# Performance work log

Hardware: AMD Instinct MI355X
Metric: run time of the kernel (lower is better)

The kernel has to match this reference:

```python
import jax, jax.numpy as jnp
import numpy as np

SG_SLOPE = 20.0  # fast_sigmoid surrogate slope
THRESHOLD = 1.0

@jax.custom_vjp
def spike_fn(v):
    # Heaviside spike with fast-sigmoid surrogate gradient
    return (v > 0).astype(v.dtype)

def _spike_fwd(v):
    return spike_fn(v), v

def _spike_bwd(v, g):
    return (g / (SG_SLOPE * jnp.abs(v) + 1.0) ** 2,)

spike_fn.defvjp(_spike_fwd, _spike_bwd)

def setup_inputs() -> dict:
    key = jax.random.key(0)
    T, IN, H, HEADS, O = 8192, 192, 1024, 5, 2
    dt = 0.004
    sp = float(np.log1p(np.exp(0.5413)))  # softplus(param) ~= 1.0
    tau_syn_h, tau_mem_h = 0.01 * sp, 0.02 * sp
    tau_syn_r = np.array([0.01, 0.02, 0.05, 0.1, 0.2]) * sp
    tau_mem_r = np.array([0.02, 0.05, 0.1, 0.2, 0.5]) * sp
    k1, k2, k3, k4 = jax.random.split(key, 4)
    x = jax.random.normal(k1, (T, IN), jnp.float32)
    W_in = jax.random.normal(k2, (H, IN), jnp.float32) / np.sqrt(IN)
    V = jax.random.normal(k3, (H, H), jnp.float32) / np.sqrt(H)
    b_rec = jnp.zeros((H,), jnp.float32)
    W_out = jax.random.normal(k4, (HEADS, O, H), jnp.float32) / np.sqrt(H)
    return {
        "x": x, "W_in": W_in, "V": V, "b_rec": b_rec, "W_out": W_out,
        "alpha_h": jnp.float32(np.exp(-dt / tau_syn_h)),
        "beta_h": jnp.float32(np.exp(-dt / tau_mem_h)),
        "alpha_r": jnp.asarray(np.exp(-dt / tau_syn_r), jnp.float32),
        "beta_r": jnp.asarray(np.exp(-dt / tau_mem_r), jnp.float32),
    }

def reference(x, W_in, V, b_rec, W_out, alpha_h, beta_h, alpha_r, beta_r):
    H = W_in.shape[0]
    HEADS, O, _ = W_out.shape
    dt_f32 = x.dtype

    def step(carry, x_t):
        inp_prev, spk, syn_h, mem_h, syn_r, mem_r = carry
        # hidden RSynaptic (note: fc_hidden consumes the PREVIOUS input, one-step delay)
        cur = W_in @ inp_prev + V @ spk + b_rec
        syn_h_new = alpha_h * syn_h + cur
        reset = jax.lax.stop_gradient(spk)  # zero-reset uses previous spike, detached
        mem_h_new = (beta_h * mem_h + syn_h_new) * (1.0 - reset)
        spk_new = spike_fn(mem_h_new - THRESHOLD)
        # readout heads consume the PREVIOUS hidden spike (pre-update)
        r_in = jnp.einsum("hoc,c->ho", W_out, spk)  # [HEADS, 2]
        syn_r_new = alpha_r[:, None] * syn_r + r_in
        mem_r_new = beta_r[:, None] * mem_r + syn_r_new  # reset_mechanism='none'
        out = mem_r_new.mean(axis=0)  # average over readout heads
        return (x_t, spk_new, syn_h_new, mem_h_new, syn_r_new, mem_r_new), out

    init = (
        jnp.zeros_like(x[0]),
        jnp.zeros((H,), dt_f32),
        jnp.zeros((H,), dt_f32),
        jnp.zeros((H,), dt_f32),
        jnp.zeros((HEADS, O), dt_f32),
        jnp.zeros((HEADS, O), dt_f32),
    )
    _, preds = jax.lax.scan(step, init, x)
    return preds  # [T, 2]
```

## Files before the change

kernel.cpp:

```cpp
#include <hip/hip_runtime.h>
#include <hip/hip_bf16.h>


constexpr int T_STEPS = 8192;
constexpr int IN_DIM  = 192;
constexpr int H_DIM   = 1024;
constexpr int NBLK    = 32;
constexpr int RING    = 4;

__global__ void k_clear(unsigned int* __restrict__ p, int n) {
    int i = blockIdx.x * blockDim.x + threadIdx.x;
    if (i < n) p[i] = 0u;
}

__global__ __launch_bounds__(576, 1) void k_phase1(
    const float* __restrict__ x,
    const float* __restrict__ W_in,
    const float* __restrict__ V,
    const float* __restrict__ b_rec,
    const float* __restrict__ alpha_h_p,
    const float* __restrict__ beta_h_p,
    unsigned long long* __restrict__ mbox,
    uint2* __restrict__ raster)
{
    const int tid   = threadIdx.x;
    const int blk   = blockIdx.x;
    const int w     = tid >> 6;
    const int l     = tid & 63;
    const bool syncw = (w == 8);
    const int r_local = l >> 4;
    const int cg      = l & 15;
    const int row   = (blk << 5) + (w << 2) + r_local;

    __shared__ unsigned int       bits_lds[RING][NBLK];
    __shared__ unsigned long long combine[2];
    __shared__ unsigned long long rdyPack;

    for (int i = tid; i < RING * NBLK; i += 576)
        ((unsigned int*)bits_lds)[i] = 0u;
    if (tid == 0) { combine[0] = 0ull; combine[1] = 0ull; rdyPack = 0ull; }

    unsigned int* rp = (unsigned int*)&rdyPack;

    float4 vfrag[16];
    float  wfrag[12];
    float  b_r = 0.f;
    if (!syncw) {
        const float4* vp = (const float4*)(V + (size_t)row * H_DIM + cg * 64);
        #pragma unroll
        for (int i = 0; i < 16; ++i) vfrag[i] = vp[i];
        const float* wp = W_in + row * IN_DIM + cg * 12;
        #pragma unroll
        for (int i = 0; i < 12; ++i) wfrag[i] = wp[i];
        b_r = b_rec[row];
    }
    const float ah = alpha_h_p[0];
    const float bh = beta_h_p[0];

    __syncthreads();

    float u0 = 1.02f, u1 = 1.03f, u2 = 1.05f, u3 = 1.07f;
    const float bc = 1.0000001f, bd = 1e-30f;

    if (syncw) {
        const bool act = (l < NBLK) && (l != blk);
        for (int t = 0; t < T_STEPS - 1; ++t) {
            const unsigned int want = (unsigned int)(t + 1);
            const unsigned long long good =
                ((unsigned long long)want << 16) | ((unsigned long long)want << 48);
            const unsigned long long* p =
                &mbox[(size_t)(((t & (RING - 1)) * NBLK + blk) * NBLK + l)];
            unsigned long long vv = act
                ? __hip_atomic_load(p, __ATOMIC_RELAXED, __HIP_MEMORY_SCOPE_AGENT)
                : good;
            bool ok = (((vv >> 16) & 0xffffull) == want) && ((vv >> 48) == want);
            while (__any(!ok)) {
                if (!ok)
                    vv = __hip_atomic_load(p, __ATOMIC_RELAXED,
                                           __HIP_MEMORY_SCOPE_AGENT);
                #pragma unroll
                for (int i = 0; i < 8; ++i) {
                    u0 = fmaf(u0, bc, bd); u1 = fmaf(u1, bc, bd);
                    u2 = fmaf(u2, bc, bd); u3 = fmaf(u3, bc, bd);
                }
                ok = (((vv >> 16) & 0xffffull) == want) && ((vv >> 48) == want);
            }
            if (act)
                bits_lds[t & (RING - 1)][l] =
                    (unsigned int)(vv & 0xffffull)
                    | ((unsigned int)((vv >> 32) & 0xffffull) << 16);
            if (l == 0)
                __hip_atomic_store(&rp[0], (unsigned int)(t + 1),
                                   __ATOMIC_RELEASE, __HIP_MEMORY_SCOPE_WORKGROUP);
        }
    } else {
        const float* xptr = x + cg * 12;
        float xr[12];
        #pragma unroll
        for (int i = 0; i < 12; ++i) xr[i] = 0.0f;
        float syn = 0.f, mem = 0.f, prev = 0.f;

        for (int t = 0; t < T_STEPS; ++t) {
            const float4* xp4 = (const float4*)xptr;
            float4 f0 = xp4[0], f1 = xp4[1], f2 = xp4[2];

            unsigned long long rv = __hip_atomic_load(&rdyPack, __ATOMIC_ACQUIRE,
                                        __HIP_MEMORY_SCOPE_WORKGROUP);
            while ((unsigned int)rv < (unsigned int)t ||
                   (unsigned int)(rv >> 32) < (unsigned int)t) {
                #pragma unroll
                for (int i = 0; i < 4; ++i) {
                    u0 = fmaf(u0, bc, bd); u1 = fmaf(u1, bc, bd);
                    u2 = fmaf(u2, bc, bd); u3 = fmaf(u3, bc, bd);
                }
                rv = __hip_atomic_load(&rdyPack, __ATOMIC_ACQUIRE,
                                       __HIP_MEMORY_SCOPE_WORKGROUP);
            }

            const int slot = (t + RING - 1) & (RING - 1);
            unsigned int b0 = bits_lds[slot][2 * cg];
            unsigned int b1 = bits_lds[slot][2 * cg + 1];

            float a0 = 0.f, a1 = 0.f;
            #pragma unroll
            for (int i = 0; i < 8; ++i) {
                a0 = fmaf((float)((b0 >> (4 * i + 0)) & 1u), vfrag[i].x, a0);
                a0 = fmaf((float)((b0 >> (4 * i + 1)) & 1u), vfrag[i].y, a0);
                a0 = fmaf((float)((b0 >> (4 * i + 2)) & 1u), vfrag[i].z, a0);
                a0 = fmaf((float)((b0 >> (4 * i + 3)) & 1u), vfrag[i].w, a0);
                a1 = fmaf((float)((b1 >> (4 * i + 0)) & 1u), vfrag[8 + i].x, a1);
                a1 = fmaf((float)((b1 >> (4 * i + 1)) & 1u), vfrag[8 + i].y, a1);
                a1 = fmaf((float)((b1 >> (4 * i + 2)) & 1u), vfrag[8 + i].z, a1);
                a1 = fmaf((float)((b1 >> (4 * i + 3)) & 1u), vfrag[8 + i].w, a1);
            }
            #pragma unroll
            for (int i = 0; i < 12; ++i) a0 = fmaf(wfrag[i], xr[i], a0);
            float acc = a0 + a1;

            #pragma unroll
            for (int m = 1; m < 16; m <<= 1) acc += __shfl_xor(acc, m, 64);

            float cur = acc + b_r;
            syn = fmaf(ah, syn, cur);
            mem = fmaf(bh, mem, syn) * (1.0f - prev);
            float spk = (mem > 1.0f) ? 1.0f : 0.0f;
            prev = spk;

            unsigned long long bal = __ballot(spk > 0.5f);
            unsigned int isLast = 0u, bitsAll = 0u;
            if (l == 0) {
                unsigned int nib = (unsigned int)(bal & 1ull)
                                 | ((unsigned int)((bal >> 16) & 1ull) << 1)
                                 | ((unsigned int)((bal >> 32) & 1ull) << 2)
                                 | ((unsigned int)((bal >> 48) & 1ull) << 3);
                unsigned long long add =
                    (1ull << 32) | ((unsigned long long)nib << (4 * w));
                unsigned long long old = __hip_atomic_fetch_add(&combine[t & 1],
                        add, __ATOMIC_RELAXED, __HIP_MEMORY_SCOPE_WORKGROUP);
                unsigned long long nv = old + add;
                if ((nv >> 32) == 8ull) { isLast = 1u; bitsAll = (unsigned int)nv; }
            }
            isLast = __shfl(isLast, 0, 64);
            if (isLast) {
                unsigned int bits = __shfl(bitsAll, 0, 64);
                unsigned int want = (unsigned int)(t + 1);
                unsigned int w0t = (want << 16) | (bits & 0xffffu);
                unsigned int w1t = (want << 16) | (bits >> 16);
                unsigned long long pack =
                    (unsigned long long)w0t | ((unsigned long long)w1t << 32);
                if (l < NBLK && l != blk) {
                    __hip_atomic_store(
                        &mbox[(size_t)(((t & (RING - 1)) * NBLK + l) * NBLK + blk)],
                        pack, __ATOMIC_RELAXED, __HIP_MEMORY_SCOPE_AGENT);
                }
                if (l == 0) {
                    raster[(size_t)t * NBLK + blk] = make_uint2(w0t, w1t);
                    bits_lds[t & (RING - 1)][blk] = bits;
                    combine[t & 1] = 0ull;
                    __hip_atomic_store(&rp[1], (unsigned int)(t + 1),
                                       __ATOMIC_RELEASE,
                                       __HIP_MEMORY_SCOPE_WORKGROUP);
                }
            }

            #pragma unroll
            for (int i = 0; i < 4; ++i) {
                xr[i]     = (&f0.x)[i];
                xr[4 + i] = (&f1.x)[i];
                xr[8 + i] = (&f2.x)[i];
            }
            xptr += IN_DIM;
        }
    }
    asm volatile("" :: "v"(u0), "v"(u1), "v"(u2), "v"(u3));
}

__global__ __launch_bounds__(256, 1) void k_readout_mm(
    const uint2* __restrict__ raster,
    const float* __restrict__ W_out,
    float* __restrict__ R)
{
    __shared__ float wlds[10 * 1033];
    for (int i = threadIdx.x; i < 10 * 1024; i += 256) {
        int r = i >> 10, c = i & 1023;
        wlds[r * 1033 + c] = W_out[i];
    }
    __syncthreads();

    int tid = threadIdx.x;
    if (tid >= 250) return;
    int tl = tid / 10, rowr = tid - tl * 10;
    int t = blockIdx.x * 25 + tl;
    if (t >= T_STEPS) return;

    float acc = 0.f;
    if (t > 0) {
        const uint2* wp = raster + (size_t)(t - 1) * NBLK;
        const float* wr = &wlds[rowr * 1033];
        for (int ww = 0; ww < NBLK; ++ww) {
            uint2 v = wp[ww];
            unsigned int bits = (v.x & 0xffffu) | ((v.y & 0xffffu) << 16);
            const float* wb = wr + ww * 32;
            #pragma unroll
            for (int j = 0; j < 32; ++j)
                acc = fmaf((float)((bits >> j) & 1u), wb[j], acc);
        }
    }
    R[t * 10 + rowr] = acc;
}

__global__ void k_scan(const float* __restrict__ R,
                       const float* __restrict__ alpha_r,
                       const float* __restrict__ beta_r,
                       float* __restrict__ memr_all)
{
    int lane = threadIdx.x;
    bool act = lane < 10;
    float a = act ? alpha_r[lane >> 1] : 0.f;
    float b = act ? beta_r[lane >> 1] : 0.f;
    float syn = 0.f, mem = 0.f;
    constexpr int PF = 8;
    float buf[PF];
    #pragma unroll
    for (int i = 0; i < PF; ++i) buf[i] = act ? R[i * 10 + lane] : 0.f;

    for (int tb = 0; tb < T_STEPS; tb += PF) {
        #pragma unroll
        for (int i = 0; i < PF; ++i) {
            int t = tb + i;
            syn = fmaf(a, syn, buf[i]);
            mem = fmaf(b, mem, syn);
            if (act) memr_all[t * 10 + lane] = mem;
            int tn = t + PF;
            buf[i] = (act && tn < T_STEPS) ? R[tn * 10 + lane] : 0.f;
        }
    }
}

__global__ void k_mean(const float* __restrict__ memr_all, float* __restrict__ out) {
    int g = blockIdx.x * blockDim.x + threadIdx.x;
    if (g >= T_STEPS * 2) return;
    int t = g >> 1, o = g & 1;
    const float* m = memr_all + t * 10 + o;
    out[g] = 0.2f * (m[0] + m[2] + m[4] + m[6] + m[8]);
}

extern "C" void kernel_launch(void* const* d_in, const int* in_sizes, int n_in,
                              void* d_out, int out_size, void* d_ws, size_t ws_size,
                              hipStream_t stream) {
    (void)in_sizes; (void)n_in; (void)out_size; (void)ws_size;
    const float* x       = (const float*)d_in[0];
    const float* W_in    = (const float*)d_in[1];
    const float* V       = (const float*)d_in[2];
    const float* b_rec   = (const float*)d_in[3];
    const float* W_out   = (const float*)d_in[4];
    const float* alpha_h = (const float*)d_in[5];
    const float* beta_h  = (const float*)d_in[6];
    const float* alpha_r = (const float*)d_in[7];
    const float* beta_r  = (const float*)d_in[8];
    float* out = (float*)d_out;

    char* wsb = (char*)d_ws;
    unsigned long long* mbox = (unsigned long long*)wsb;
    uint2* raster  = (uint2*)(wsb + RING * NBLK * NBLK * 8);
    float* Rbuf    = (float*)(wsb + RING * NBLK * NBLK * 8
                              + (size_t)T_STEPS * NBLK * 8);
    float* memr_all = Rbuf + (size_t)T_STEPS * 10;

    int nclr = RING * NBLK * NBLK * 2;
    k_clear<<<(nclr + 255) / 256, 256, 0, stream>>>((unsigned int*)mbox, nclr);
    k_phase1<<<NBLK, 576, 0, stream>>>(x, W_in, V, b_rec, alpha_h, beta_h,
                                       mbox, raster);
    k_readout_mm<<<(T_STEPS + 24) / 25, 256, 0, stream>>>(raster, W_out, Rbuf);
    k_scan<<<1, 64, 0, stream>>>(Rbuf, alpha_r, beta_r, memr_all);
    k_mean<<<(T_STEPS * 2 + 255) / 256, 256, 0, stream>>>(memr_all, out);
}
```

Baseline: 17.78 ms.

## Add dummy spinning blocks for clock boost and pipeline mailbox polling loads

Launches 256 blocks instead of 32. The extra 224 blocks do busy FMA work until the worker blocks set a done flag, apparently to keep the GPU clocks high or the power state active during the latency-bound recurrence. The sync wavefront now keeps four relaxed mailbox loads in flight and uses warp-wide __all exits instead of serial reload-and-spin. Worker blocks also raise their scheduling priority and do less dummy FMA work while waiting. This risks extra power draw and contention, and could deadlock if the 32 worker blocks are not all resident together.

```diff
diff --git a/kernel.cpp b/kernel.cpp
--- a/kernel.cpp
+++ b/kernel.cpp
@@ -7,6 +7,15 @@
 constexpr int H_DIM   = 1024;
 constexpr int NBLK    = 32;
 constexpr int RING    = 4;
+constexpr int NGRID   = 256;
+
+#define LOADP() __hip_atomic_load(pa, __ATOMIC_RELAXED, __HIP_MEMORY_SCOPE_AGENT)
+#define GOOD(v) ((((unsigned int)((v) >> 16) & 0xffffu) == want) && \
+                 ((unsigned int)((v) >> 48) == want))
+#define POLL_STEP(ri) \
+    if (!ok && GOOD(ri)) { word = ri; ok = true; } \
+    if (__all(ok)) break; \
+    ri = LOADP();
 
 __global__ void k_clear(unsigned int* __restrict__ p, int n) {
     int i = blockIdx.x * blockDim.x + threadIdx.x;
@@ -21,10 +30,36 @@
     const float* __restrict__ alpha_h_p,
     const float* __restrict__ beta_h_p,
     unsigned long long* __restrict__ mbox,
+    unsigned int* __restrict__ doneFlag,
     uint2* __restrict__ raster)
 {
-    const int tid   = threadIdx.x;
-    const int blk   = blockIdx.x;
+    const int tid = threadIdx.x;
+    const int blk = blockIdx.x;
+    const float bc = 1.0000001f, bd = 1e-30f;
+
+    if (blk >= NBLK) {
+        __shared__ volatile int exitf;
+        if (tid == 0) exitf = 0;
+        __syncthreads();
+        float u0 = 1.02f, u1 = 1.03f, u2 = 1.05f, u3 = 1.07f;
+        const unsigned int* df = &doneFlag[(blk & 31) << 4];
+        for (;;) {
+            #pragma unroll 8
+            for (int i = 0; i < 192; ++i) {
+                u0 = fmaf(u0, bc, bd); u1 = fmaf(u1, bc, bd);
+                u2 = fmaf(u2, bc, bd); u3 = fmaf(u3, bc, bd);
+            }
+            if (tid == 0 &&
+                __hip_atomic_load(df, __ATOMIC_RELAXED, __HIP_MEMORY_SCOPE_AGENT))
+                exitf = 1;
+            if (exitf) break;
+        }
+        asm volatile("" :: "v"(u0), "v"(u1), "v"(u2), "v"(u3));
+        return;
+    }
+
+    __builtin_amdgcn_s_setprio(1);
+
     const int w     = tid >> 6;
     const int l     = tid & 63;
     const bool syncw = (w == 8);
@@ -39,7 +74,6 @@
     for (int i = tid; i < RING * NBLK; i += 576)
         ((unsigned int*)bits_lds)[i] = 0u;
     if (tid == 0) { combine[0] = 0ull; combine[1] = 0ull; rdyPack = 0ull; }
-
     unsigned int* rp = (unsigned int*)&rdyPack;
 
     float4 vfrag[16];
@@ -59,36 +93,30 @@
 
     __syncthreads();
 
-    float u0 = 1.02f, u1 = 1.03f, u2 = 1.05f, u3 = 1.07f;
-    const float bc = 1.0000001f, bd = 1e-30f;
+    float u0 = 1.02f, u1 = 1.03f;
 
     if (syncw) {
         const bool act = (l < NBLK) && (l != blk);
         for (int t = 0; t < T_STEPS - 1; ++t) {
             const unsigned int want = (unsigned int)(t + 1);
-            const unsigned long long good =
+            const unsigned long long* pa =
+                &mbox[((size_t)(t & (RING - 1)) * NBLK + blk) * NBLK + (l & 31)];
+            unsigned long long word =
                 ((unsigned long long)want << 16) | ((unsigned long long)want << 48);
-            const unsigned long long* p =
-                &mbox[(size_t)(((t & (RING - 1)) * NBLK + blk) * NBLK + l)];
-            unsigned long long vv = act
-                ? __hip_atomic_load(p, __ATOMIC_RELAXED, __HIP_MEMORY_SCOPE_AGENT)
-                : good;
-            bool ok = (((vv >> 16) & 0xffffull) == want) && ((vv >> 48) == want);
-            while (__any(!ok)) {
-                if (!ok)
-                    vv = __hip_atomic_load(p, __ATOMIC_RELAXED,
-                                           __HIP_MEMORY_SCOPE_AGENT);
-                #pragma unroll
-                for (int i = 0; i < 8; ++i) {
-                    u0 = fmaf(u0, bc, bd); u1 = fmaf(u1, bc, bd);
-                    u2 = fmaf(u2, bc, bd); u3 = fmaf(u3, bc, bd);
-                }
-                ok = (((vv >> 16) & 0xffffull) == want) && ((vv >> 48) == want);
+            bool ok = !act;
+            unsigned long long r0 = LOADP(), r1 = LOADP(),
+                               r2 = LOADP(), r3 = LOADP();
+            for (;;) {
+                POLL_STEP(r0)
+                POLL_STEP(r1)
+                POLL_STEP(r2)
+                POLL_STEP(r3)
+                u0 = fmaf(u0, bc, bd); u1 = fmaf(u1, bc, bd);
             }
             if (act)
                 bits_lds[t & (RING - 1)][l] =
-                    (unsigned int)(vv & 0xffffull)
-                    | ((unsigned int)((vv >> 32) & 0xffffull) << 16);
+                    (unsigned int)(word & 0xffffull)
+                    | ((unsigned int)((word >> 32) & 0xffffull) << 16);
             if (l == 0)
                 __hip_atomic_store(&rp[0], (unsigned int)(t + 1),
                                    __ATOMIC_RELEASE, __HIP_MEMORY_SCOPE_WORKGROUP);
@@ -108,11 +136,7 @@
                                         __HIP_MEMORY_SCOPE_WORKGROUP);
             while ((unsigned int)rv < (unsigned int)t ||
                    (unsigned int)(rv >> 32) < (unsigned int)t) {
-                #pragma unroll
-                for (int i = 0; i < 4; ++i) {
-                    u0 = fmaf(u0, bc, bd); u1 = fmaf(u1, bc, bd);
-                    u2 = fmaf(u2, bc, bd); u3 = fmaf(u3, bc, bd);
-                }
+                u0 = fmaf(u0, bc, bd); u1 = fmaf(u1, bc, bd);
                 rv = __hip_atomic_load(&rdyPack, __ATOMIC_ACQUIRE,
                                        __HIP_MEMORY_SCOPE_WORKGROUP);
             }
@@ -170,7 +194,7 @@
                     (unsigned long long)w0t | ((unsigned long long)w1t << 32);
                 if (l < NBLK && l != blk) {
                     __hip_atomic_store(
-                        &mbox[(size_t)(((t & (RING - 1)) * NBLK + l) * NBLK + blk)],
+                        &mbox[((size_t)(t & (RING - 1)) * NBLK + l) * NBLK + blk],
                         pack, __ATOMIC_RELAXED, __HIP_MEMORY_SCOPE_AGENT);
                 }
                 if (l == 0) {
@@ -192,7 +216,11 @@
             xptr += IN_DIM;
         }
     }
-    asm volatile("" :: "v"(u0), "v"(u1), "v"(u2), "v"(u3));
+    asm volatile("" :: "v"(u0), "v"(u1));
+
+    if (tid == 0)
+        __hip_atomic_store(&doneFlag[blk << 4], 1u,
+                           __ATOMIC_RELAXED, __HIP_MEMORY_SCOPE_AGENT);
 }
 
 __global__ __launch_bounds__(256, 1) void k_readout_mm(
@@ -282,15 +310,16 @@
 
     char* wsb = (char*)d_ws;
     unsigned long long* mbox = (unsigned long long*)wsb;
-    uint2* raster  = (uint2*)(wsb + RING * NBLK * NBLK * 8);
-    float* Rbuf    = (float*)(wsb + RING * NBLK * NBLK * 8
+    unsigned int* doneFlag = (unsigned int*)(wsb + RING * NBLK * NBLK * 8);
+    uint2* raster  = (uint2*)(wsb + RING * NBLK * NBLK * 8 + 2048);
+    float* Rbuf    = (float*)(wsb + RING * NBLK * NBLK * 8 + 2048
                               + (size_t)T_STEPS * NBLK * 8);
     float* memr_all = Rbuf + (size_t)T_STEPS * 10;
 
-    int nclr = RING * NBLK * NBLK * 2;
+    int nclr = RING * NBLK * NBLK * 2 + 512;
     k_clear<<<(nclr + 255) / 256, 256, 0, stream>>>((unsigned int*)mbox, nclr);
-    k_phase1<<<NBLK, 576, 0, stream>>>(x, W_in, V, b_rec, alpha_h, beta_h,
-                                       mbox, raster);
+    k_phase1<<<NGRID, 576, 0, stream>>>(x, W_in, V, b_rec, alpha_h, beta_h,
+                                        mbox, doneFlag, raster);
     k_readout_mm<<<(T_STEPS + 24) / 25, 256, 0, stream>>>(raster, W_out, Rbuf);
     k_scan<<<1, 64, 0, stream>>>(Rbuf, alpha_r, beta_r, memr_all);
     k_mean<<<(T_STEPS * 2 + 255) / 256, 256, 0, stream>>>(memr_all, out);
```

After: 19.85 ms. +11.6%, slower.
